# Optimization experiments

Hardware: AMD Instinct MI355X
Metric: run time of the kernel (lower is better)

The kernel has to match this reference:

```python
import jax, jax.numpy as jnp
import numpy as np

EPS = 1e-5
DIL = 2
PAD = 2  # dilation * (kernel_size - 1) // 2


def _conv(x, w, dil, pad):
    return jax.lax.conv_general_dilated(
        x, w, window_strides=(1, 1), padding=[(pad, pad), (pad, pad)],
        rhs_dilation=(dil, dil), dimension_numbers=('NCHW', 'OIHW', 'NCHW'))


def _bn(x, g, b):
    # BatchNorm2d in training mode: per-channel batch stats over (N,H,W)
    m = x.mean(axis=(0, 2, 3), keepdims=True)
    v = x.var(axis=(0, 2, 3), keepdims=True)
    return (x - m) * jax.lax.rsqrt(v + EPS) * g[None, :, None, None] + b[None, :, None, None]


def _deform_conv(x, offset, w, dil=DIL, pad=PAD):
    # torchvision deform_conv2d v1 (no modulation): offset [B, 2*K, H, W] with
    # channel ordering (dy_0, dx_0, dy_1, dx_1, ...), kernel tap k = ky*3 + kx.
    B, C, H, W = x.shape
    Co = w.shape[0]
    K = 9
    off = offset.reshape(B, K, 2, H, W)
    dy, dx = off[:, :, 0], off[:, :, 1]              # [B,K,H,W]
    kr = jnp.arange(3)
    kyy = (jnp.repeat(kr, 3) * dil - pad).astype(x.dtype)   # [K]
    kxx = (jnp.tile(kr, 3) * dil - pad).astype(x.dtype)     # [K]
    hg = jnp.arange(H, dtype=x.dtype)
    wg = jnp.arange(W, dtype=x.dtype)
    py = hg[None, None, :, None] + kyy[None, :, None, None] + dy   # [B,K,H,W]
    px = wg[None, None, None, :] + kxx[None, :, None, None] + dx   # [B,K,H,W]
    y0 = jnp.floor(py)
    x0 = jnp.floor(px)
    wy = py - y0   # [B,K,H,W]
    wx = px - x0
    y0i = y0.astype(jnp.int32)
    x0i = x0.astype(jnp.int32)
    x_flat = x.reshape(B, C, H * W)

    def corner(yi, xi):
        valid = ((yi >= 0) & (yi < H) & (xi >= 0) & (xi < W)).astype(x.dtype)  # [B,K,H,W]
        idx = jnp.clip(yi, 0, H - 1) * W + jnp.clip(xi, 0, W - 1)
        v = jax.vmap(lambda xb, ib: xb[:, ib])(x_flat, idx.reshape(B, -1))    # [B,C,K*H*W]
        return v.reshape(B, C, K, H, W) * valid[:, None]

    v00 = corner(y0i, x0i)
    v01 = corner(y0i, x0i + 1)
    v10 = corner(y0i + 1, x0i)
    v11 = corner(y0i + 1, x0i + 1)
    wy_ = wy[:, None]   # [B,1,K,H,W]
    wx_ = wx[:, None]
    sampled = (v00 * (1 - wy_) * (1 - wx_) + v01 * (1 - wy_) * wx_
               + v10 * wy_ * (1 - wx_) + v11 * wy_ * wx_)          # [B,C,K,H,W]
    return jnp.einsum('bckhw,ock->bohw', sampled, w.reshape(Co, C, K))


def setup_inputs() -> dict:
    key = jax.random.key(0)
    ks = jax.random.split(key, 4)
    B, C, H, W = 4, 256, 56, 56
    x = jax.random.normal(ks[0], (B, C, H, W), dtype=jnp.float32)
    w_off = jax.random.normal(ks[1], (18, C, 3, 3), dtype=jnp.float32) * 0.01
    b_off = jnp.zeros((18,), dtype=jnp.float32)
    w1 = jax.random.normal(ks[2], (C, C, 3, 3), dtype=jnp.float32) * (1.0 / np.sqrt(9 * C))
    w2 = jax.random.normal(ks[3], (C, C, 3, 3), dtype=jnp.float32) * (1.0 / np.sqrt(9 * C))
    gamma1 = jnp.ones((C,), dtype=jnp.float32)
    beta1 = jnp.zeros((C,), dtype=jnp.float32)
    gamma2 = jnp.ones((C,), dtype=jnp.float32)
    beta2 = jnp.zeros((C,), dtype=jnp.float32)
    return {'x': x, 'w_off': w_off, 'b_off': b_off, 'w1': w1, 'gamma1': gamma1,
            'beta1': beta1, 'w2': w2, 'gamma2': gamma2, 'beta2': beta2}


def reference(x, w_off, b_off, w1, gamma1, beta1, w2, gamma2, beta2):
    offset = _conv(x, w_off, DIL, PAD) + b_off[None, :, None, None]   # [B,18,H,W]
    out = _deform_conv(x, offset, w1)
    out = jax.nn.relu(_bn(out, gamma1, beta1))
    out = _conv(out, w2, 1, 1)
    out = _bn(out, gamma2, beta2)
    return jax.nn.relu(out + x)
```

## Files before the change

### kernel.cpp

```cpp
#include <hip/hip_runtime.h>

typedef __bf16 bf16;
typedef bf16 bf16x4 __attribute__((ext_vector_type(4)));
typedef bf16 bf16x8 __attribute__((ext_vector_type(8)));
typedef float f32x4 __attribute__((ext_vector_type(4)));

#define CH 256
#define HH 56
#define WW 56
#define HW 3136
#define MM 12544
#define KT 2304

__device__ __forceinline__ void gll16(const bf16* g, bf16* l) {
  __builtin_amdgcn_global_load_lds(
      (const __attribute__((address_space(1))) void*)g,
      (__attribute__((address_space(3))) void*)l, 16, 0, 0);
}

template <int N>
__device__ __forceinline__ void waitvm() {
  if constexpr (N == 0) asm volatile("s_waitcnt vmcnt(0)" ::: "memory");
  else if constexpr (N == 3) asm volatile("s_waitcnt vmcnt(3)" ::: "memory");
  else if constexpr (N == 4) asm volatile("s_waitcnt vmcnt(4)" ::: "memory");
}

__global__ __launch_bounds__(256) void nchw2nhwc_k(const float* __restrict__ x,
                                                   bf16* __restrict__ o) {
  __shared__ float t[32][33];
  const int b = blockIdx.z, hw0 = blockIdx.x * 32, c0 = blockIdx.y * 32;
  const int tid = threadIdx.x;
  {
    const int cl = tid >> 3, hwl = (tid & 7) * 4;
    f32x4 v = *(const f32x4*)&x[(size_t)(b * CH + c0 + cl) * HW + hw0 + hwl];
#pragma unroll
    for (int i = 0; i < 4; ++i) t[cl][hwl + i] = v[i];
  }
  __syncthreads();
  const int hwl = tid >> 3, cl = (tid & 7) * 4;
  bf16x4 ov;
#pragma unroll
  for (int i = 0; i < 4; ++i) ov[i] = (bf16)t[cl + i][hwl];
  *(bf16x4*)&o[(size_t)(b * HW + hw0 + hwl) * CH + c0 + cl] = ov;
}

__global__ void reorder_all_k(const float* __restrict__ w1,
                              const float* __restrict__ w2,
                              const float* __restrict__ woff,
                              bf16* __restrict__ w1t, bf16* __restrict__ w2t,
                              bf16* __restrict__ wof) {
  const int gid = blockIdx.x;
  if (gid < 4608) {
    const int idx = gid * 256 + threadIdx.x;
    const float* in = (gid < 2304) ? w1 : w2;
    bf16* out = (gid < 2304) ? w1t : w2t;
    const int li = (gid < 2304) ? idx : idx - 2304 * 256;
    const int o = li / KT, r = li - o * KT;
    const int k = r >> 8, c = r & 255;
    out[li] = (bf16)in[(size_t)(o * CH + c) * 9 + k];
  } else {
    const int li = (gid - 4608) * 256 + threadIdx.x;
    const int o = li / KT, r = li - o * KT;
    const int k = r >> 8, c = r & 255;
    wof[li] = (bf16)((o < 18) ? woff[(size_t)(o * CH + c) * 9 + k] : 0.f);
  }
}

__global__ __launch_bounds__(256) void build_deform_k(
    const bf16* __restrict__ xn, const float* __restrict__ offb,
    const float* __restrict__ boff, bf16* __restrict__ A1) {
  const int tid = threadIdx.x;
  const int m = blockIdx.x * 16 + (tid >> 4);
  const int l15 = tid & 15;
  const int b = m / HW, hw = m - b * HW;
  const int h = hw / WW, w = hw - h * WW;
  const float* orow = offb + m * 18;
  const bf16* xb = xn + (size_t)b * HW * CH;
  bf16* dst = A1 + (size_t)m * KT;
  for (int tap = 0; tap < 9; ++tap) {
    const int ky = tap / 3, kx = tap - ky * 3;
    const float dy = orow[2 * tap] + boff[2 * tap];
    const float dx = orow[2 * tap + 1] + boff[2 * tap + 1];
    const float py = (float)(h + ky * 2 - 2) + dy;
    const float px = (float)(w + kx * 2 - 2) + dx;
    const float y0f = floorf(py), x0f = floorf(px);
    const int y0 = (int)y0f, x0 = (int)x0f;
    const float wy = py - y0f, wx = px - x0f;
    const float w00 = (1.f - wy) * (1.f - wx), w01 = (1.f - wy) * wx;
    const float w10 = wy * (1.f - wx), w11 = wy * wx;
    const bool vy0 = (unsigned)y0 < HH, vy1 = (unsigned)(y0 + 1) < HH;
    const bool vx0 = (unsigned)x0 < WW, vx1 = (unsigned)(x0 + 1) < WW;
    const bf16* p00 = xb + (long long)(y0 * WW + x0) * CH;
#pragma unroll
    for (int j = 0; j < 2; ++j) {
      const int cc = j * 128 + l15 * 8;
      bf16x8 v00 = {}, v01 = {}, v10 = {}, v11 = {};
      if (vy0 && vx0) v00 = *(const bf16x8*)(p00 + cc);
      if (vy0 && vx1) v01 = *(const bf16x8*)(p00 + CH + cc);
      if (vy1 && vx0) v10 = *(const bf16x8*)(p00 + WW * CH + cc);
      if (vy1 && vx1) v11 = *(const bf16x8*)(p00 + WW * CH + CH + cc);
      bf16x8 o;
#pragma unroll
      for (int i = 0; i < 8; ++i)
        o[i] = (bf16)(w00 * (float)v00[i] + w01 * (float)v01[i] +
                      w10 * (float)v10[i] + w11 * (float)v11[i]);
      *(bf16x8*)(dst + tap * 256 + cc) = o;
    }
  }
}

template <int MODE, int EPI, int SWZ, int TN, int KS>
__global__ __launch_bounds__(256, 3) void gemm_k(
    const bf16* __restrict__ Asrc, const bf16* __restrict__ Bt,
    const bf16* __restrict__ zp, bf16* __restrict__ outb,
    float* __restrict__ sS, float* __restrict__ sQ,
    float* __restrict__ offout, const int dil, const int pad) {
  constexpr int PB = TN / 32;
  constexpr int NF = TN / 32;
  constexpr int SL = 2 + PB;
  __shared__ __align__(16) bf16 Ab[2][4096];
  __shared__ __align__(16) bf16 Bb[2][TN * 64];
  const int tid = threadIdx.x;
  int n0, m0;
  if (SWZ) {
    const int gid = blockIdx.x;
    const int swz = (gid & 7) * 98 + (gid >> 3);
    n0 = (swz & 3) * 64;
    m0 = (swz >> 2) * 64;
  } else {
    n0 = blockIdx.x * TN;
    m0 = blockIdx.y * 64;
  }
  const int kbase = blockIdx.z * KS * 64;
  const int lane = tid & 63, wv = tid >> 6;
  const int wrM = wv >> 1, wcN = wv & 1;
  const int fr = lane & 15, kg = lane >> 4;
  const int srow = tid >> 3, cpos = tid & 7;
  const int sxor = (cpos ^ (srow & 7)) * 8;

  int bb[2], hh[2], wwv[2];
  const bf16* aptr[2];
  if (MODE == 1) {
#pragma unroll
    for (int pa = 0; pa < 2; ++pa) {
      const int m = m0 + pa * 32 + srow;
      bb[pa] = m / HW;
      const int hw = m - bb[pa] * HW;
      hh[pa] = hw / WW;
      wwv[pa] = hw - hh[pa] * WW;
    }
  } else {
#pragma unroll
    for (int pa = 0; pa < 2; ++pa)
      aptr[pa] = Asrc + (size_t)(m0 + pa * 32 + srow) * KT + kbase + sxor;
  }
  const bf16* bptr[PB];
#pragma unroll
  for (int pb = 0; pb < PB; ++pb)
    bptr[pb] = Bt + (size_t)(n0 + pb * 32 + srow) * KT + kbase + sxor;

  f32x4 acc[2][NF] = {};

  auto STAGE = [&](int kt, int buf) {
    const int kk = kbase + kt * 64;
#pragma unroll
    for (int pa = 0; pa < 2; ++pa) {
      const bf16* as;
      if (MODE == 0) {
        as = aptr[pa] + kt * 64;
      } else {
        const int tap = kk >> 8, coff = kk & 255;
        const int ky = tap / 3, kx = tap - ky * 3;
        const int y = hh[pa] + ky * dil - pad, xx = wwv[pa] + kx * dil - pad;
        const bool ok = ((unsigned)y < HH) && ((unsigned)xx < WW);
        as = ok ? Asrc + ((size_t)(bb[pa] * HW + y * WW + xx) * CH + coff + sxor)
                : zp + sxor;
      }
      gll16(as, &Ab[buf][(pa * 32 + srow) * 64 + cpos * 8]);
    }
#pragma unroll
    for (int pb = 0; pb < PB; ++pb)
      gll16(bptr[pb] + kt * 64, &Bb[buf][(pb * 32 + srow) * 64 + cpos * 8]);
  };

  auto COMPUTE = [&](int buf) {
#pragma unroll
    for (int kh = 0; kh < 2; ++kh) {
      bf16x8 af[2], bv[NF];
#pragma unroll
      for (int mf = 0; mf < 2; ++mf) {
        const int row = wrM * 32 + mf * 16 + fr;
        const int g = (kh * 4 + kg) ^ (row & 7);
        af[mf] = *(const bf16x8*)&Ab[buf][row * 64 + g * 8];
      }
#pragma unroll
      for (int nf = 0; nf < NF; ++nf) {
        const int row = wcN * (NF * 16) + nf * 16 + fr;
        const int g = (kh * 4 + kg) ^ (row & 7);
        bv[nf] = *(const bf16x8*)&Bb[buf][row * 64 + g * 8];
      }
#pragma unroll
      for (int mf = 0; mf < 2; ++mf)
#pragma unroll
        for (int nf = 0; nf < NF; ++nf)
          acc[mf][nf] = __builtin_amdgcn_mfma_f32_16x16x32_bf16(af[mf], bv[nf],
                                                                acc[mf][nf], 0, 0, 0);
    }
  };

  STAGE(0, 0);
  STAGE(1, 1);
  int buf = 0;
  for (int kt = 0; kt < KS; ++kt) {
    if (kt + 1 < KS) waitvm<SL>();
    else waitvm<0>();
    __builtin_amdgcn_s_barrier();
    __builtin_amdgcn_sched_barrier(0);
    COMPUTE(buf);
    __builtin_amdgcn_sched_barrier(0);
    __builtin_amdgcn_s_barrier();
    if (kt + 2 < KS) STAGE(kt + 2, buf);
    buf ^= 1;
  }

  if constexpr (EPI == 1) {
#pragma unroll
    for (int mf = 0; mf < 2; ++mf) {
      const int rr = m0 + wrM * 32 + mf * 16 + kg * 4;
#pragma unroll
      for (int nf = 0; nf < NF; ++nf) {
        const int col = n0 + wcN * (NF * 16) + nf * 16 + fr;
#pragma unroll
        for (int r = 0; r < 4; ++r)
          outb[(size_t)(rr + r) * CH + col] = (bf16)acc[mf][nf][r];
      }
    }
    float ps[NF], pq[NF];
#pragma unroll
    for (int nf = 0; nf < NF; ++nf) {
      float s = 0.f, q = 0.f;
#pragma unroll
      for (int mf = 0; mf < 2; ++mf)
#pragma unroll
        for (int r = 0; r < 4; ++r) {
          const float v = acc[mf][nf][r];
          s += v;
          q += v * v;
        }
      s += __shfl_xor(s, 16);
      s += __shfl_xor(s, 32);
      q += __shfl_xor(q, 16);
      q += __shfl_xor(q, 32);
      ps[nf] = s;
      pq[nf] = q;
    }
    float* red = (float*)&Ab[0][0];
    if (tid < 128) red[tid] = 0.f;
    __syncthreads();
    if (kg == 0) {
#pragma unroll
      for (int nf = 0; nf < NF; ++nf) {
        const int cb = wcN * (NF * 16) + nf * 16 + fr;
        atomicAdd(&red[cb], ps[nf]);
        atomicAdd(&red[64 + cb], pq[nf]);
      }
    }
    __syncthreads();
    if (tid < 64) {
      atomicAdd(&sS[n0 + tid], red[tid]);
      atomicAdd(&sQ[n0 + tid], red[64 + tid]);
    }
  } else {
#pragma unroll
    for (int mf = 0; mf < 2; ++mf) {
      const int rr = m0 + wrM * 32 + mf * 16 + kg * 4;
#pragma unroll
      for (int nf = 0; nf < NF; ++nf) {
        const int col = n0 + wcN * (NF * 16) + nf * 16 + fr;
        if (col < 18) {
#pragma unroll
          for (int r = 0; r < 4; ++r)
            atomicAdd(&offout[(size_t)(rr + r) * 18 + col], acc[mf][nf][r]);
        }
      }
    }
  }
}

__global__ __launch_bounds__(256) void a1_kb(const bf16* __restrict__ in,
                                             const float* __restrict__ s,
                                             const float* __restrict__ sq,
                                             const float* __restrict__ g,
                                             const float* __restrict__ be,
                                             bf16* __restrict__ out) {
  const size_t idx = (size_t)(blockIdx.x * 256 + threadIdx.x) * 8;
  const int c0 = (int)(idx & 255);
  const float inv = 1.f / (float)MM;
  bf16x8 v = *(const bf16x8*)&in[idx];
  bf16x8 o;
#pragma unroll
  for (int i = 0; i < 8; ++i) {
    const int c = c0 + i;
    const float mean = s[c] * inv;
    const float var = sq[c] * inv - mean * mean;
    const float sc = g[c] * rsqrtf(var + 1e-5f);
    const float bi = be[c] - mean * sc;
    float r = (float)v[i] * sc + bi;
    o[i] = (bf16)(r > 0.f ? r : 0.f);
  }
  *(bf16x8*)&out[idx] = o;
}

__global__ __launch_bounds__(256) void final_kb(const bf16* __restrict__ o2,
                                                const float* __restrict__ x,
                                                const float* __restrict__ s,
                                                const float* __restrict__ sq,
                                                const float* __restrict__ g,
                                                const float* __restrict__ be,
                                                float* __restrict__ out) {
  __shared__ float t[32][33];
  const int b = blockIdx.z, hw0 = blockIdx.x * 32, o0 = blockIdx.y * 32;
  const int tid = threadIdx.x;
  {
    const int hwl = tid >> 3, ol = (tid & 7) * 4;
    bf16x4 v = *(const bf16x4*)&o2[(size_t)(b * HW + hw0 + hwl) * CH + o0 + ol];
#pragma unroll
    for (int i = 0; i < 4; ++i) t[ol + i][hwl] = (float)v[i];
  }
  __syncthreads();
  const int ol = tid >> 3, hwl = (tid & 7) * 4;
  const int ch = o0 + ol;
  const float inv = 1.f / (float)MM;
  const float mean = s[ch] * inv;
  const float var = sq[ch] * inv - mean * mean;
  const float sc = g[ch] * rsqrtf(var + 1e-5f);
  const float bb = be[ch] - mean * sc;
  const size_t xi = (size_t)(b * CH + ch) * HW + hw0 + hwl;
  f32x4 xv = *(const f32x4*)&x[xi];
  f32x4 r;
#pragma unroll
  for (int i = 0; i < 4; ++i) {
    float v = t[ol][hwl + i] * sc + bb + xv[i];
    r[i] = v > 0.f ? v : 0.f;
  }
  *(f32x4*)&out[xi] = r;
}

#define WS_XN 0ULL
#define WS_W1T 6422528ULL
#define WS_W2T 7602176ULL
#define WS_WOF 8781824ULL
#define WS_OFFB 9076736ULL
#define WS_A1 9979904ULL
#define WS_O1 67782656ULL
#define WS_ACT 74205184ULL
#define WS_O2 80627712ULL
#define WS_ZP 87050240ULL
#define WS_STAT 87054336ULL

extern "C" void kernel_launch(void* const* d_in, const int* in_sizes, int n_in,
                              void* d_out, int out_size, void* d_ws, size_t ws_size,
                              hipStream_t stream) {
  const float* x = (const float*)d_in[0];
  const float* w_off = (const float*)d_in[1];
  const float* b_off = (const float*)d_in[2];
  const float* w1 = (const float*)d_in[3];
  const float* g1 = (const float*)d_in[4];
  const float* be1 = (const float*)d_in[5];
  const float* w2 = (const float*)d_in[6];
  const float* g2 = (const float*)d_in[7];
  const float* be2 = (const float*)d_in[8];
  float* out = (float*)d_out;
  char* ws = (char*)d_ws;

  bf16* xn = (bf16*)(ws + WS_XN);
  bf16* w1t = (bf16*)(ws + WS_W1T);
  bf16* w2t = (bf16*)(ws + WS_W2T);
  bf16* wof = (bf16*)(ws + WS_WOF);
  float* offb = (float*)(ws + WS_OFFB);
  bf16* A1 = (bf16*)(ws + WS_A1);
  bf16* o1 = (bf16*)(ws + WS_O1);
  bf16* act = (bf16*)(ws + WS_ACT);
  bf16* o2 = (bf16*)(ws + WS_O2);
  bf16* zp = (bf16*)(ws + WS_ZP);
  float* s1 = (float*)(ws + WS_STAT);
  float* sq1 = (float*)(ws + WS_STAT + 1024);
  float* s2 = (float*)(ws + WS_STAT + 2048);
  float* sq2 = (float*)(ws + WS_STAT + 3072);

  hipMemsetAsync(ws + WS_ZP, 0, 8192, stream);
  hipMemsetAsync(ws + WS_OFFB, 0, 903168, stream);

  nchw2nhwc_k<<<dim3(98, 8, 4), 256, 0, stream>>>(x, xn);
  reorder_all_k<<<5184, 256, 0, stream>>>(w1, w2, w_off, w1t, w2t, wof);

  gemm_k<1, 0, 0, 32, 9><<<dim3(1, 196, 4), 256, 0, stream>>>(
      xn, wof, zp, nullptr, nullptr, nullptr, offb, 2, 2);

  build_deform_k<<<784, 256, 0, stream>>>(xn, offb, b_off, A1);

  gemm_k<0, 1, 1, 64, 36><<<dim3(784), 256, 0, stream>>>(
      A1, w1t, zp, o1, s1, sq1, nullptr, 0, 0);
  a1_kb<<<1568, 256, 0, stream>>>(o1, s1, sq1, g1, be1, act);

  gemm_k<1, 1, 1, 64, 36><<<dim3(784), 256, 0, stream>>>(
      act, w2t, zp, o2, s2, sq2, nullptr, 1, 1);

  final_kb<<<dim3(98, 8, 4), 256, 0, stream>>>(o2, x, s2, sq2, g2, be2, out);
}
```

Measured before the change: 203.9 us.

## Load GEMM B operand directly into registers, bypassing LDS staging

The weight (B) tile no longer goes through shared memory. Each wave loads its MFMA B fragments straight from global memory into a register double buffer one k-step ahead, while the A tile keeps its double-buffered LDS path. This removes the B LDS writes and reads and cuts LDS footprint per block. In exchange, waves sharing columns fetch B redundantly from global/L2, register pressure rises, and the load latency is hidden by only one compute step.

```diff
diff --git a/kernel.cpp b/kernel.cpp
--- a/kernel.cpp
+++ b/kernel.cpp
@@ -21,8 +21,7 @@
 template <int N>
 __device__ __forceinline__ void waitvm() {
   if constexpr (N == 0) asm volatile("s_waitcnt vmcnt(0)" ::: "memory");
-  else if constexpr (N == 3) asm volatile("s_waitcnt vmcnt(3)" ::: "memory");
-  else if constexpr (N == 4) asm volatile("s_waitcnt vmcnt(4)" ::: "memory");
+  else if constexpr (N == 2) asm volatile("s_waitcnt vmcnt(2)" ::: "memory");
 }
 
 __global__ __launch_bounds__(256) void nchw2nhwc_k(const float* __restrict__ x,
@@ -115,11 +114,8 @@
     const bf16* __restrict__ zp, bf16* __restrict__ outb,
     float* __restrict__ sS, float* __restrict__ sQ,
     float* __restrict__ offout, const int dil, const int pad) {
-  constexpr int PB = TN / 32;
   constexpr int NF = TN / 32;
-  constexpr int SL = 2 + PB;
   __shared__ __align__(16) bf16 Ab[2][4096];
-  __shared__ __align__(16) bf16 Bb[2][TN * 64];
   const int tid = threadIdx.x;
   int n0, m0;
   if (SWZ) {
@@ -154,14 +150,16 @@
     for (int pa = 0; pa < 2; ++pa)
       aptr[pa] = Asrc + (size_t)(m0 + pa * 32 + srow) * KT + kbase + sxor;
   }
-  const bf16* bptr[PB];
-#pragma unroll
-  for (int pb = 0; pb < PB; ++pb)
-    bptr[pb] = Bt + (size_t)(n0 + pb * 32 + srow) * KT + kbase + sxor;
+  const bf16* bfp[NF];
+#pragma unroll
+  for (int nf = 0; nf < NF; ++nf)
+    bfp[nf] = Bt + (size_t)(n0 + wcN * (NF * 16) + nf * 16 + fr) * KT + kbase +
+              kg * 8;
 
   f32x4 acc[2][NF] = {};
-
-  auto STAGE = [&](int kt, int buf) {
+  bf16x8 bvbuf[2][NF][2];
+
+  auto STAGEA = [&](int kt, int buf) {
     const int kk = kbase + kt * 64;
 #pragma unroll
     for (int pa = 0; pa < 2; ++pa) {
@@ -178,15 +176,20 @@
       }
       gll16(as, &Ab[buf][(pa * 32 + srow) * 64 + cpos * 8]);
     }
-#pragma unroll
-    for (int pb = 0; pb < PB; ++pb)
-      gll16(bptr[pb] + kt * 64, &Bb[buf][(pb * 32 + srow) * 64 + cpos * 8]);
   };
 
-  auto COMPUTE = [&](int buf) {
+  auto LOADB = [&](int kt, int p) {
+#pragma unroll
+    for (int nf = 0; nf < NF; ++nf)
+#pragma unroll
+      for (int kh = 0; kh < 2; ++kh)
+        bvbuf[p][nf][kh] = *(const bf16x8*)(bfp[nf] + kt * 64 + kh * 32);
+  };
+
+  auto COMPUTE = [&](int buf, int p) {
 #pragma unroll
     for (int kh = 0; kh < 2; ++kh) {
-      bf16x8 af[2], bv[NF];
+      bf16x8 af[2];
 #pragma unroll
       for (int mf = 0; mf < 2; ++mf) {
         const int row = wrM * 32 + mf * 16 + fr;
@@ -194,33 +197,28 @@
         af[mf] = *(const bf16x8*)&Ab[buf][row * 64 + g * 8];
       }
 #pragma unroll
-      for (int nf = 0; nf < NF; ++nf) {
-        const int row = wcN * (NF * 16) + nf * 16 + fr;
-        const int g = (kh * 4 + kg) ^ (row & 7);
-        bv[nf] = *(const bf16x8*)&Bb[buf][row * 64 + g * 8];
-      }
-#pragma unroll
       for (int mf = 0; mf < 2; ++mf)
 #pragma unroll
         for (int nf = 0; nf < NF; ++nf)
-          acc[mf][nf] = __builtin_amdgcn_mfma_f32_16x16x32_bf16(af[mf], bv[nf],
-                                                                acc[mf][nf], 0, 0, 0);
+          acc[mf][nf] = __builtin_amdgcn_mfma_f32_16x16x32_bf16(
+              af[mf], bvbuf[p][nf][kh], acc[mf][nf], 0, 0, 0);
     }
   };
 
-  STAGE(0, 0);
-  STAGE(1, 1);
-  int buf = 0;
+  LOADB(0, 0);
+  STAGEA(0, 0);
+  STAGEA(1, 1);
+#pragma unroll 2
   for (int kt = 0; kt < KS; ++kt) {
-    if (kt + 1 < KS) waitvm<SL>();
+    if (kt + 1 < KS) waitvm<2>();
     else waitvm<0>();
     __builtin_amdgcn_s_barrier();
     __builtin_amdgcn_sched_barrier(0);
-    COMPUTE(buf);
+    if (kt + 1 < KS) LOADB(kt + 1, (kt + 1) & 1);
+    COMPUTE(kt & 1, kt & 1);
     __builtin_amdgcn_sched_barrier(0);
     __builtin_amdgcn_s_barrier();
-    if (kt + 2 < KS) STAGE(kt + 2, buf);
-    buf ^= 1;
+    if (kt + 2 < KS) STAGEA(kt + 2, kt & 1);
   }
 
   if constexpr (EPI == 1) {
```

After: 300.4 us. 47.4% more time.
